# Kernel optimization log

Hardware: AMD Instinct MI355X
Metric: run time of the kernel (lower is better)

The kernel has to match this reference:

```python
import jax, jax.numpy as jnp
import numpy as np

B = 4096      # graphs
N = 21        # nodes per graph (EEG electrodes)
CIN = 512
H1 = 1024
H2 = 1024
COUT = 512
R = 4         # SE reduction
RANK = 10     # nodevec rank
EPS = 1e-5
THRESH = 0.1


def setup_inputs() -> dict:
    key = jax.random.key(0)
    ks = jax.random.split(key, 16)
    p = lambda i, shape, s=0.02: (jax.random.normal(ks[i], shape, jnp.float32) * s)
    return {
        "x": jax.random.normal(ks[0], (B * N, CIN), jnp.float32),
        "batch": jnp.arange(B * N, dtype=jnp.int32) // N,
        "nodevec1": jax.random.normal(ks[1], (N, RANK), jnp.float32),
        "nodevec2": jax.random.normal(ks[2], (RANK, N), jnp.float32),
        "se_w1": p(3, (CIN, CIN // R), 0.05),
        "se_w2": p(4, (CIN // R, CIN), 0.05),
        "W1": p(5, (CIN, H1)), "b1": jnp.zeros((H1,), jnp.float32),
        "W2": p(6, (H1, H2)), "b2": jnp.zeros((H2,), jnp.float32),
        "W3": p(7, (H2, COUT)), "b3": jnp.zeros((COUT,), jnp.float32),
        "bn1_g": jnp.ones((H1,), jnp.float32), "bn1_b": jnp.zeros((H1,), jnp.float32),
        "bn2_g": jnp.ones((H2,), jnp.float32), "bn2_b": jnp.zeros((H2,), jnp.float32),
        "bn3_g": jnp.ones((COUT,), jnp.float32), "bn3_b": jnp.zeros((COUT,), jnp.float32),
        "rs1_w": p(8, (CIN, H1)), "rs1_b": jnp.zeros((H1,), jnp.float32),
        "fc_w": p(9, (COUT, 2 * COUT)), "fc_b": jnp.zeros((2 * COUT,), jnp.float32),
    }


def _batchnorm(h, g, b):
    # training-mode BN: biased batch stats over the node dimension
    m = h.mean(0)
    v = h.var(0)
    return (h - m) * jax.lax.rsqrt(v + EPS) * g + b


def _gcn(A, h, W, b):
    # GCNConv with precomputed normalized+thresholded weights:
    # out = A_block_diag @ (h @ W) + b, done densely per graph since A is 21x21
    hm = (h @ W).reshape(B, N, -1)                 # [B, N, Cout]
    agg = jnp.einsum('ij,bjc->bic', A, hm)         # message passing per graph
    return agg.reshape(B * N, -1) + b


def _forward(x, batch, nodevec1, nodevec2, se_w1, se_w2,
             W1, b1, W2, b2, W3, b3,
             bn1_g, bn1_b, bn2_g, bn2_b, bn3_g, bn3_b,
             rs1_w, rs1_b, fc_w, fc_b):
    # SE layer on [B, N, C]: channel-wise gating from node-mean features
    x3 = x.reshape(B, N, CIN)
    y = jax.nn.sigmoid(jax.nn.relu(x3.mean(1) @ se_w1) @ se_w2)   # [B, C]
    xg = (x3 * y[:, None, :]).reshape(B * N, CIN)
    # adaptive adjacency: sigmoid(nv1 @ nv2), symmetric normalize, threshold
    adp = jax.nn.sigmoid(nodevec1 @ nodevec2)                      # [N, N]
    at = adp + jnp.eye(N, dtype=adp.dtype)
    deg = at.sum(1)
    dinv = jnp.where(deg > 0, deg ** -0.5, 0.0)
    A = dinv[:, None] * at * dinv[None, :]
    A = jnp.where(A > THRESH, A, 0.0)
    # layer 1 (+ projected residual, BN, relu; dropout omitted = eval)
    h = _batchnorm(_gcn(A, xg, W1, b1), bn1_g, bn1_b) + (xg @ rs1_w + rs1_b)
    h = jax.nn.relu(h)
    # layer 2 (h1 == h2 -> identity residual)
    h = jax.nn.relu(_batchnorm(_gcn(A, h, W2, b2), bn2_g, bn2_b) + h)
    # layer 3
    h = _batchnorm(_gcn(A, h, W3, b3), bn3_g, bn3_b)
    # global mean pool by graph id
    ssum = jax.ops.segment_sum(h, batch, num_segments=B)
    cnt = jax.ops.segment_sum(jnp.ones((h.shape[0], 1), h.dtype), batch, num_segments=B)
    pooled = ssum / cnt
    return pooled @ fc_w + fc_b                                    # [B, 2*COUT]


def reference(x, batch, nodevec1, nodevec2, se_w1, se_w2,
              W1, b1, W2, b2, W3, b3,
              bn1_g, bn1_b, bn2_g, bn2_b, bn3_g, bn3_b,
              rs1_w, rs1_b, fc_w, fc_b):
    return _forward(x, batch, nodevec1, nodevec2, se_w1, se_w2,
                    W1, b1, W2, b2, W3, b3,
                    bn1_g, bn1_b, bn2_g, bn2_b, bn3_g, bn3_b,
                    rs1_w, rs1_b, fc_w, fc_b)
```

## Files before the change

### kernel.cpp

```cpp
#include <hip/hip_runtime.h>

typedef _Float16 f16;
typedef f16 f16x2 __attribute__((ext_vector_type(2)));
typedef f16 f16x4 __attribute__((ext_vector_type(4)));
typedef f16 f16x8 __attribute__((ext_vector_type(8)));
typedef float f32x4 __attribute__((ext_vector_type(4)));
typedef const void __attribute__((address_space(1)))* gas1;
typedef void __attribute__((address_space(3)))* las3;

#define NB 4096
#define NN 21
#define MROWS (NB*NN)
#define CIN 512

__global__ void k_adj(const float* __restrict__ nv1, const float* __restrict__ nv2,
                      float* __restrict__ Aout) {
  __shared__ float at[21][21];
  __shared__ float dinv[21];
  int t = threadIdx.x;
  if (t < 441) {
    int i = t / 21, j = t % 21;
    float s = 0.f;
    #pragma unroll
    for (int r = 0; r < 10; r++) s += nv1[i*10 + r] * nv2[r*21 + j];
    float v = 1.f / (1.f + expf(-s));
    if (i == j) v += 1.f;
    at[i][j] = v;
  }
  __syncthreads();
  if (t < 21) {
    float d = 0.f;
    #pragma unroll
    for (int j = 0; j < 21; j++) d += at[t][j];
    dinv[t] = d > 0.f ? rsqrtf(d) : 0.f;
  }
  __syncthreads();
  if (t < 441) {
    int i = t / 21, j = t % 21;
    float a = dinv[i] * at[i][j] * dinv[j];
    Aout[t] = a > 0.1f ? a : 0.f;
  }
}

__global__ void k_transpose(const float* __restrict__ src, f16* __restrict__ dst,
                            int K, int N) {
  __shared__ float tile[32][33];
  int n0 = blockIdx.x * 32, k0 = blockIdx.y * 32;
  int tx = threadIdx.x, ty = threadIdx.y;
  #pragma unroll
  for (int i = 0; i < 4; i++)
    tile[ty + 8*i][tx] = src[(size_t)(k0 + ty + 8*i) * N + n0 + tx];
  __syncthreads();
  #pragma unroll
  for (int i = 0; i < 4; i++)
    dst[(size_t)(n0 + ty + 8*i) * K + k0 + tx] = (f16)tile[tx][ty + 8*i];
}

__global__ void k_mean(const float* __restrict__ x, float* __restrict__ xm) {
  int b = blockIdx.x, t = threadIdx.x;
  for (int c = t; c < CIN; c += 256) {
    float s = 0.f;
    #pragma unroll
    for (int n = 0; n < NN; n++) s += x[((size_t)b*NN + n)*CIN + c];
    xm[(size_t)b*CIN + c] = s * (1.f/21.f);
  }
}

__global__ void k_se1(const float* __restrict__ xm, const float* __restrict__ w1,
                      float* __restrict__ y1) {
  __shared__ float row[CIN];
  int b = blockIdx.x, t = threadIdx.x;
  for (int k = t; k < CIN; k += 128) row[k] = xm[(size_t)b*CIN + k];
  __syncthreads();
  float acc = 0.f;
  for (int k = 0; k < CIN; k++) acc += row[k] * w1[(size_t)k*128 + t];
  y1[(size_t)b*128 + t] = fmaxf(acc, 0.f);
}

__global__ void k_se2(const float* __restrict__ y1, const float* __restrict__ w2,
                      float* __restrict__ y) {
  __shared__ float row[128];
  int b = blockIdx.x, t = threadIdx.x;
  if (t < 128) row[t] = y1[(size_t)b*128 + t];
  __syncthreads();
  float acc = 0.f;
  for (int k = 0; k < 128; k++) acc += row[k] * w2[(size_t)k*CIN + t];
  y[(size_t)b*CIN + t] = 1.f / (1.f + expf(-acc));
}

__global__ void k_gate(const float* __restrict__ x, const float* __restrict__ y,
                       f16* __restrict__ xg) {
  size_t i8 = (size_t)blockIdx.x * 256 + threadIdx.x;
  size_t base = i8 * 8;
  int r = (int)(base >> 9);
  int c = (int)(base & 511);
  int b = r / 21;
  const float4* xp = (const float4*)(x + base);
  const float4* yp = (const float4*)(y + (size_t)b*CIN + c);
  float4 a0 = xp[0], a1 = xp[1];
  float4 g0 = yp[0], g1 = yp[1];
  f16x8 o;
  o[0] = (f16)(a0.x * g0.x); o[1] = (f16)(a0.y * g0.y);
  o[2] = (f16)(a0.z * g0.z); o[3] = (f16)(a0.w * g0.w);
  o[4] = (f16)(a1.x * g1.x); o[5] = (f16)(a1.y * g1.y);
  o[6] = (f16)(a1.z * g1.z); o[7] = (f16)(a1.w * g1.w);
  *(f16x8*)(xg + base) = o;
}

#define QBUF 65536

template<int MODE>
__global__ __launch_bounds__(512, 1)
void k_gemm256(const f16* __restrict__ A, const f16* __restrict__ BT,
               f16* __restrict__ C1, const float* __restrict__ bias,
               float* __restrict__ Cf, float* __restrict__ psum,
               float* __restrict__ psq, int N, int K, int lgn) {
  __shared__ __align__(16) char lds[2 * QBUF];
  const int tid = threadIdx.x;
  const int nwg = gridDim.x;
  const int g = blockIdx.x;
  const int swz = (g & 7) * (nwg >> 3) + (g >> 3);
  const int bn = swz & ((1 << lgn) - 1);
  const int bm = swz >> lgn;
  const int lane = tid & 63;
  const int wid = tid >> 6;
  const int wr = wid >> 2;
  const int wc = wid & 3;
  const int fr = lane & 15;
  const int kg = lane >> 4;

  int srcOff[8];
  #pragma unroll
  for (int j = 0; j < 8; j++) {
    int gid = j * 512 + tid;
    int row = (gid >> 3) & 255;
    int gr = gid & 7;
    int gsw = gr ^ (row & 7);
    srcOff[j] = ((j < 4 ? bm : bn) * 256 + row) * K + gsw * 8;
  }
  const int ldsBase = tid * 16;

  const int x7 = fr & 7;
  const int aBase = (wr*128 + fr) * 128;
  const int bBase = 32768 + (wc*64 + fr) * 128;

  f32x4 acc[8][4];
  #pragma unroll
  for (int m = 0; m < 8; m++)
    #pragma unroll
    for (int n = 0; n < 4; n++)
      #pragma unroll
      for (int r = 0; r < 4; r++) acc[m][n][r] = 0.f;

  auto STAGEH = [&](int t2, int sbuf, int j0) {
    char* dst = (char*)lds + sbuf * QBUF;
    const size_t kof = (size_t)t2 * 64;
    #pragma unroll
    for (int j = j0; j < j0 + 2; j++) {
      const f16* src = (j < 4 ? A : BT) + srcOff[j] + kof;
      __builtin_amdgcn_global_load_lds((gas1)src, (las3)(dst + ldsBase + j*8192), 16, 0, 0);
    }
  };
  auto READF = [&](f16x8* av, f16x8* bv, const char* rb, int s) {
    const int ko = ((s*4 + kg) ^ x7) << 4;
    #pragma unroll
    for (int m = 0; m < 8; m++) av[m] = *(const f16x8*)(rb + aBase + m*2048 + ko);
    #pragma unroll
    for (int n = 0; n < 4; n++) bv[n] = *(const f16x8*)(rb + bBase + n*2048 + ko);
  };

  f16x8 av[8], bv[4];
  const int NT = K >> 6;
  STAGEH(0, 0, 0); STAGEH(0, 0, 2); STAGEH(0, 0, 4); STAGEH(0, 0, 6);
  asm volatile("s_waitcnt vmcnt(0)" ::: "memory");
  asm volatile("s_barrier" ::: "memory");

  for (int t = 0; t < NT; t++) {
    const char* rb = (const char*)lds + (t & 1) * QBUF;
    const int nb = (t + 1) & 1;
    const bool stg = (t + 1) < NT;

    if (stg) { STAGEH(t + 1, nb, 0); STAGEH(t + 1, nb, 2); }
    READF(av, bv, rb, 0);
    __builtin_amdgcn_s_setprio(1);
    #pragma unroll
    for (int m = 0; m < 8; m++)
      #pragma unroll
      for (int n = 0; n < 4; n++)
        acc[m][n] = __builtin_amdgcn_mfma_f32_16x16x32_f16(bv[n], av[m], acc[m][n], 0, 0, 0);
    __builtin_amdgcn_s_setprio(0);
    if (stg) { STAGEH(t + 1, nb, 4); STAGEH(t + 1, nb, 6); }
    READF(av, bv, rb, 1);
    __builtin_amdgcn_s_setprio(1);
    #pragma unroll
    for (int m = 0; m < 8; m++)
      #pragma unroll
      for (int n = 0; n < 4; n++)
        acc[m][n] = __builtin_amdgcn_mfma_f32_16x16x32_f16(bv[n], av[m], acc[m][n], 0, 0, 0);
    __builtin_amdgcn_s_setprio(0);
    if (stg) asm volatile("s_waitcnt vmcnt(0)" ::: "memory");
    asm volatile("s_barrier" ::: "memory");
  }

  const int crow = bm*256 + wr*128 + fr;
  const int ccol = bn*256 + wc*64 + kg*4;
  if constexpr (MODE == 2) {
    #pragma unroll
    for (int n = 0; n < 4; n++) {
      float4 bb = *(const float4*)(bias + ccol + n*16);
      #pragma unroll
      for (int m = 0; m < 8; m++) {
        float4 v;
        v.x = acc[m][n][0] + bb.x; v.y = acc[m][n][1] + bb.y;
        v.z = acc[m][n][2] + bb.z; v.w = acc[m][n][3] + bb.w;
        *(float4*)(Cf + (size_t)(crow + m*16) * N + ccol + n*16) = v;
      }
    }
  } else {
    #pragma unroll
    for (int m = 0; m < 8; m++)
      #pragma unroll
      for (int n = 0; n < 4; n++) {
        f16x4 o;
        o[0] = (f16)acc[m][n][0]; o[1] = (f16)acc[m][n][1];
        o[2] = (f16)acc[m][n][2]; o[3] = (f16)acc[m][n][3];
        *(f16x4*)(C1 + (size_t)(crow + m*16) * N + ccol + n*16) = o;
      }
  }
  if constexpr (MODE == 1) {
    float s[4][4], q[4][4];
    #pragma unroll
    for (int n = 0; n < 4; n++)
      #pragma unroll
      for (int r = 0; r < 4; r++) {
        float ss = 0.f, qq = 0.f;
        #pragma unroll
        for (int m = 0; m < 8; m++) { float v = acc[m][n][r]; ss += v; qq = fmaf(v, v, qq); }
        s[n][r] = ss; q[n][r] = qq;
      }
    #pragma unroll
    for (int n = 0; n < 4; n++)
      #pragma unroll
      for (int r = 0; r < 4; r++) {
        s[n][r] += __shfl_xor(s[n][r], 1); s[n][r] += __shfl_xor(s[n][r], 2);
        s[n][r] += __shfl_xor(s[n][r], 4); s[n][r] += __shfl_xor(s[n][r], 8);
        q[n][r] += __shfl_xor(q[n][r], 1); q[n][r] += __shfl_xor(q[n][r], 2);
        q[n][r] += __shfl_xor(q[n][r], 4); q[n][r] += __shfl_xor(q[n][r], 8);
      }
    float* wred = (float*)lds;
    __syncthreads();
    if (fr == 0) {
      #pragma unroll
      for (int n = 0; n < 4; n++)
        #pragma unroll
        for (int r = 0; r < 4; r++) {
          int c = wc*64 + n*16 + kg*4 + r;
          wred[wr*256 + c]       = s[n][r];
          wred[512 + wr*256 + c] = q[n][r];
        }
    }
    __syncthreads();
    if (tid < 256) {
      psum[(size_t)bm * N + bn*256 + tid] = wred[tid]       + wred[256 + tid];
      psq [(size_t)bm * N + bn*256 + tid] = wred[512 + tid] + wred[768 + tid];
    }
  }
}

__global__ __launch_bounds__(256)
void k_mixip(f16* __restrict__ t, const float* __restrict__ Aadj) {
  __shared__ float A[441];
  int b = blockIdx.x, tid = threadIdx.x;
  for (int i = tid; i < 441; i += 256) A[i] = Aadj[i];
  __syncthreads();
  int c0 = tid * 2;
  size_t base = (size_t)b * NN * 512 + c0;
  float vx[21], vy[21];
  #pragma unroll
  for (int j = 0; j < 21; j++) {
    f16x2 v = *(const f16x2*)(t + base + (size_t)j * 512);
    vx[j] = (float)v[0]; vy[j] = (float)v[1];
  }
  #pragma unroll
  for (int i = 0; i < 21; i++) {
    float a0 = 0.f, a1 = 0.f;
    #pragma unroll
    for (int j = 0; j < 21; j++) { float w = A[i*21+j]; a0 = fmaf(w, vx[j], a0); a1 = fmaf(w, vy[j], a1); }
    f16x2 o; o[0] = (f16)a0; o[1] = (f16)a1;
    *(f16x2*)(t + base + (size_t)i * 512) = o;
  }
}

__global__ __launch_bounds__(256)
void k_mix(f16* __restrict__ t, const float* __restrict__ Aadj,
           float* __restrict__ psum, float* __restrict__ psq, int C) {
  __shared__ float A[441];
  int b = blockIdx.x, tid = threadIdx.x;
  for (int i = tid; i < 441; i += 256) A[i] = Aadj[i];
  __syncthreads();
  int c0 = (blockIdx.y * 256 + tid) * 2;
  size_t base = (size_t)b * NN * C + c0;
  float vx[21], vy[21];
  #pragma unroll
  for (int j = 0; j < 21; j++) {
    f16x2 v = *(const f16x2*)(t + base + (size_t)j * C);
    vx[j] = (float)v[0]; vy[j] = (float)v[1];
  }
  float s0 = 0.f, s1 = 0.f, q0 = 0.f, q1 = 0.f;
  #pragma unroll
  for (int i = 0; i < 21; i++) {
    float a0 = 0.f, a1 = 0.f;
    #pragma unroll
    for (int j = 0; j < 21; j++) {
      float w = A[i*21 + j];
      a0 = fmaf(w, vx[j], a0);
      a1 = fmaf(w, vy[j], a1);
    }
    f16x2 o; o[0] = (f16)a0; o[1] = (f16)a1;
    *(f16x2*)(t + base + (size_t)i * C) = o;
    s0 += a0; s1 += a1;
    q0 = fmaf(a0, a0, q0); q1 = fmaf(a1, a1, q1);
  }
  float2 sv; sv.x = s0; sv.y = s1;
  float2 qv; qv.x = q0; qv.y = q1;
  *(float2*)(psum + (size_t)b * C + c0) = sv;
  *(float2*)(psq  + (size_t)b * C + c0) = qv;
}

__global__ void k_reduce(const float* __restrict__ ps, const float* __restrict__ pq,
                         float* __restrict__ rs, float* __restrict__ rq,
                         int C, int per) {
  int c = blockIdx.x * 256 + threadIdx.x;
  int py = blockIdx.y;
  float s = 0.f, q = 0.f;
  for (int p = py*per; p < py*per + per; p++) {
    s += ps[(size_t)p*C + c];
    q += pq[(size_t)p*C + c];
  }
  rs[(size_t)py*C + c] = s;
  rq[(size_t)py*C + c] = q;
}

__global__ void k_bnparams(const float* __restrict__ psum, const float* __restrict__ psq,
                           const float* __restrict__ gamma, const float* __restrict__ beta,
                           const float* __restrict__ resbias,
                           float* __restrict__ scale, float* __restrict__ shift,
                           int C, int npart) {
  int c = blockIdx.x * 256 + threadIdx.x;
  float s = 0.f, q = 0.f;
  for (int p = 0; p < npart; p++) { s += psum[(size_t)p*C + c]; q += psq[(size_t)p*C + c]; }
  const float Minv = 1.f / (float)MROWS;
  float mean = s * Minv;
  float var = q * Minv - mean * mean;
  float sc = gamma[c] * rsqrtf(var + 1e-5f);
  float sh = beta[c] - mean * sc;
  if (resbias) sh += resbias[c];
  scale[c] = sc; shift[c] = sh;
}

__global__ void k_finalize(const f16* __restrict__ g, const f16* res,
                           f16* dst, const float* __restrict__ scale,
                           const float* __restrict__ shift, int cmask) {
  size_t i8 = (size_t)blockIdx.x * 256 + threadIdx.x;
  size_t base = i8 * 8;
  int c = (int)(base & (size_t)cmask);
  f16x8 gv = *(const f16x8*)(g + base);
  f16x8 rv = *(const f16x8*)(res + base);
  f16x8 o;
  #pragma unroll
  for (int j = 0; j < 8; j++) {
    float v = (float)gv[j] * scale[c + j] + shift[c + j] + (float)rv[j];
    o[j] = (f16)fmaxf(v, 0.f);
  }
  *(f16x8*)(dst + base) = o;
}

__global__ __launch_bounds__(256)
void k_finmix(const f16* t, const f16* res, f16* hout, f16* hmix,
              const float* __restrict__ scale, const float* __restrict__ shift,
              const float* __restrict__ Aadj, int C) {
  __shared__ float A[441];
  int b = blockIdx.x, tid = threadIdx.x;
  for (int i = tid; i < 441; i += 256) A[i] = Aadj[i];
  __syncthreads();
  int c0 = (blockIdx.y * 256 + tid) * 2;
  float scx = scale[c0], scy = scale[c0+1];
  float shx = shift[c0], shy = shift[c0+1];
  size_t base = (size_t)b * NN * C + c0;
  float hx[21], hy[21];
  #pragma unroll
  for (int j = 0; j < 21; j++) {
    f16x2 tv = *(const f16x2*)(t + base + (size_t)j*C);
    f16x2 rv = *(const f16x2*)(res + base + (size_t)j*C);
    hx[j] = fmaxf((float)tv[0]*scx + shx + (float)rv[0], 0.f);
    hy[j] = fmaxf((float)tv[1]*scy + shy + (float)rv[1], 0.f);
    if (hout) {
      f16x2 o; o[0] = (f16)hx[j]; o[1] = (f16)hy[j];
      *(f16x2*)(hout + base + (size_t)j*C) = o;
    }
  }
  #pragma unroll
  for (int i = 0; i < 21; i++) {
    float a0 = 0.f, a1 = 0.f;
    #pragma unroll
    for (int j = 0; j < 21; j++) { float w = A[i*21+j]; a0 = fmaf(w, hx[j], a0); a1 = fmaf(w, hy[j], a1); }
    f16x2 o; o[0] = (f16)a0; o[1] = (f16)a1;
    *(f16x2*)(hmix + base + (size_t)i*C) = o;
  }
}

__global__ void k_pool(const f16* __restrict__ g3, const float* __restrict__ scale,
                       const float* __restrict__ shift, f16* __restrict__ pooled) {
  int b = blockIdx.x, t = threadIdx.x;
  for (int c = t; c < 512; c += 256) {
    float s = 0.f;
    #pragma unroll
    for (int n = 0; n < NN; n++) s += (float)g3[((size_t)b*NN + n)*512 + c];
    pooled[(size_t)b*512 + c] = (f16)((s * (1.f/21.f)) * scale[c] + shift[c]);
  }
}

extern "C" void kernel_launch(void* const* d_in, const int* in_sizes, int n_in,
                              void* d_out, int out_size, void* d_ws, size_t ws_size,
                              hipStream_t stream) {
  const float* x     = (const float*)d_in[0];
  const float* nv1   = (const float*)d_in[2];
  const float* nv2   = (const float*)d_in[3];
  const float* se_w1 = (const float*)d_in[4];
  const float* se_w2 = (const float*)d_in[5];
  const float* W1    = (const float*)d_in[6];
  const float* W2    = (const float*)d_in[8];
  const float* W3    = (const float*)d_in[10];
  const float* bn1g  = (const float*)d_in[12];
  const float* bn1b  = (const float*)d_in[13];
  const float* bn2g  = (const float*)d_in[14];
  const float* bn2b  = (const float*)d_in[15];
  const float* bn3g  = (const float*)d_in[16];
  const float* bn3b  = (const float*)d_in[17];
  const float* rs1w  = (const float*)d_in[18];
  const float* rs1b  = (const float*)d_in[19];
  const float* fcw   = (const float*)d_in[20];
  const float* fcb   = (const float*)d_in[21];
  float* out = (float*)d_out;

  char* ws = (char*)d_ws;
  size_t off = 0;
  auto alloc = [&](size_t bytes) -> char* {
    char* p = ws + off;
    off = (off + bytes + 255) & ~(size_t)255;
    return p;
  };

  float* A_adj = (float*)alloc(441 * 4);
  f16* W1T  = (f16*)alloc((size_t)1024 * 512 * 2);
  f16* RS1T = (f16*)alloc((size_t)1024 * 512 * 2);
  f16* W2T  = (f16*)alloc((size_t)1024 * 1024 * 2);
  f16* W3T  = (f16*)alloc((size_t)512 * 1024 * 2);
  f16* FCWT = (f16*)alloc((size_t)1024 * 512 * 2);
  float* psum = (float*)alloc((size_t)NB * 1024 * 4);
  float* psq  = (float*)alloc((size_t)NB * 1024 * 4);
  float* y1   = (float*)alloc((size_t)NB * 128 * 4);
  float* rsum = (float*)alloc((size_t)32 * 1024 * 4);
  float* rsq  = (float*)alloc((size_t)32 * 1024 * 4);
  float* sc1 = (float*)alloc(1024 * 4);
  float* sh1 = (float*)alloc(1024 * 4);
  float* sc2 = (float*)alloc(1024 * 4);
  float* sh2 = (float*)alloc(1024 * 4);
  float* sc3 = (float*)alloc(1024 * 4);
  float* sh3 = (float*)alloc(1024 * 4);
  f16* pooled = (f16*)alloc((size_t)NB * 512 * 2);
  f16* G = (f16*)alloc((size_t)MROWS * 512 * 2);
  f16* R = (f16*)alloc((size_t)MROWS * 1024 * 2);
  f16* T = (f16*)alloc((size_t)MROWS * 1024 * 2);
  float* xm = psum;
  float* yv = psq;
  (void)ws_size; (void)in_sizes; (void)n_in; (void)out_size;

  k_adj<<<1, 512, 0, stream>>>(nv1, nv2, A_adj);
  k_transpose<<<dim3(32, 16), dim3(32, 8), 0, stream>>>(W1,   W1T,  512, 1024);
  k_transpose<<<dim3(32, 16), dim3(32, 8), 0, stream>>>(rs1w, RS1T, 512, 1024);
  k_transpose<<<dim3(32, 32), dim3(32, 8), 0, stream>>>(W2,   W2T,  1024, 1024);
  k_transpose<<<dim3(16, 32), dim3(32, 8), 0, stream>>>(W3,   W3T,  1024, 512);
  k_transpose<<<dim3(32, 16), dim3(32, 8), 0, stream>>>(fcw,  FCWT, 512, 1024);

  k_mean<<<NB, 256, 0, stream>>>(x, xm);
  k_se1<<<NB, 128, 0, stream>>>(xm, se_w1, y1);
  k_se2<<<NB, 512, 0, stream>>>(y1, se_w2, yv);
  k_gate<<<21504, 256, 0, stream>>>(x, yv, G);

  k_gemm256<0><<<1344, 512, 0, stream>>>(G, RS1T, R, nullptr, nullptr, nullptr, nullptr, 1024, 512, 2);
  k_mixip<<<NB, 256, 0, stream>>>(G, A_adj);
  k_gemm256<1><<<1344, 512, 0, stream>>>(G, W1T, T, nullptr, nullptr, psum, psq, 1024, 512, 2);
  k_reduce<<<dim3(4, 24), 256, 0, stream>>>(psum, psq, rsum, rsq, 1024, 14);
  k_bnparams<<<4, 256, 0, stream>>>(rsum, rsq, bn1g, bn1b, rs1b, sc1, sh1, 1024, 24);
  k_finalize<<<43008, 256, 0, stream>>>(T, R, R, sc1, sh1, 1023);

  k_gemm256<0><<<1344, 512, 0, stream>>>(R, W2T, T, nullptr, nullptr, nullptr, nullptr, 1024, 1024, 2);
  k_mix<<<dim3(NB, 2), 256, 0, stream>>>(T, A_adj, psum, psq, 1024);
  k_reduce<<<dim3(4, 32), 256, 0, stream>>>(psum, psq, rsum, rsq, 1024, 128);
  k_bnparams<<<4, 256, 0, stream>>>(rsum, rsq, bn2g, bn2b, nullptr, sc2, sh2, 1024, 32);
  k_finmix<<<dim3(NB, 2), 256, 0, stream>>>(T, R, nullptr, T, sc2, sh2, A_adj, 1024);

  k_gemm256<1><<<672, 512, 0, stream>>>(T, W3T, G, nullptr, nullptr, psum, psq, 512, 1024, 1);
  k_reduce<<<dim3(2, 24), 256, 0, stream>>>(psum, psq, rsum, rsq, 512, 14);
  k_bnparams<<<2, 256, 0, stream>>>(rsum, rsq, bn3g, bn3b, nullptr, sc3, sh3, 512, 24);

  k_pool<<<NB, 256, 0, stream>>>(G, sc3, sh3, pooled);
  k_gemm256<2><<<64, 512, 0, stream>>>(pooled, FCWT, nullptr, fcb, out, nullptr, nullptr, 1024, 512, 2);
}
```

Baseline: 1.180 ms.

## Fuse SE mean/MLP/gate into one kernel and batch weight transposes

Replaces the four SE kernels (mean, two small MLP layers, gate) with one kernel that processes 8 graphs per block. Per-graph means and MLP activations stay in shared memory, and the w1/w2 weight loads are shared across the 8 graphs. The five weight-transpose launches become a single launch that picks its matrix by block index. For layers 1 and 3, the separate reduce step is dropped and the BN-parameter kernel sums all 336 partials directly, which cuts launches but makes each of only 2–4 blocks do a long serial loop. The SE kernel reads x twice and runs only 512 blocks, so occupancy may be lower.

```diff
diff --git a/kernel.cpp b/kernel.cpp
--- a/kernel.cpp
+++ b/kernel.cpp
@@ -42,10 +42,22 @@
   }
 }
 
-__global__ void k_transpose(const float* __restrict__ src, f16* __restrict__ dst,
-                            int K, int N) {
+__global__ void k_transpose_all(const float* __restrict__ s0, const float* __restrict__ s1,
+                                const float* __restrict__ s2, const float* __restrict__ s3,
+                                const float* __restrict__ s4,
+                                f16* __restrict__ d0, f16* __restrict__ d1,
+                                f16* __restrict__ d2, f16* __restrict__ d3,
+                                f16* __restrict__ d4) {
   __shared__ float tile[32][33];
-  int n0 = blockIdx.x * 32, k0 = blockIdx.y * 32;
+  int b = blockIdx.x;
+  const float* src; f16* dst; int K, N, local;
+  if (b < 512)       { src = s0; dst = d0; K = 512;  N = 1024; local = b; }
+  else if (b < 1024) { src = s1; dst = d1; K = 512;  N = 1024; local = b - 512; }
+  else if (b < 2048) { src = s2; dst = d2; K = 1024; N = 1024; local = b - 1024; }
+  else if (b < 2560) { src = s3; dst = d3; K = 1024; N = 512;  local = b - 2048; }
+  else               { src = s4; dst = d4; K = 512;  N = 1024; local = b - 2560; }
+  int ntn = N >> 5;
+  int n0 = (local % ntn) * 32, k0 = (local / ntn) * 32;
   int tx = threadIdx.x, ty = threadIdx.y;
   #pragma unroll
   for (int i = 0; i < 4; i++)
@@ -56,55 +68,74 @@
     dst[(size_t)(n0 + ty + 8*i) * K + k0 + tx] = (f16)tile[tx][ty + 8*i];
 }
 
-__global__ void k_mean(const float* __restrict__ x, float* __restrict__ xm) {
-  int b = blockIdx.x, t = threadIdx.x;
-  for (int c = t; c < CIN; c += 256) {
-    float s = 0.f;
-    #pragma unroll
-    for (int n = 0; n < NN; n++) s += x[((size_t)b*NN + n)*CIN + c];
-    xm[(size_t)b*CIN + c] = s * (1.f/21.f);
-  }
-}
-
-__global__ void k_se1(const float* __restrict__ xm, const float* __restrict__ w1,
-                      float* __restrict__ y1) {
-  __shared__ float row[CIN];
-  int b = blockIdx.x, t = threadIdx.x;
-  for (int k = t; k < CIN; k += 128) row[k] = xm[(size_t)b*CIN + k];
-  __syncthreads();
-  float acc = 0.f;
-  for (int k = 0; k < CIN; k++) acc += row[k] * w1[(size_t)k*128 + t];
-  y1[(size_t)b*128 + t] = fmaxf(acc, 0.f);
-}
-
-__global__ void k_se2(const float* __restrict__ y1, const float* __restrict__ w2,
-                      float* __restrict__ y) {
-  __shared__ float row[128];
-  int b = blockIdx.x, t = threadIdx.x;
-  if (t < 128) row[t] = y1[(size_t)b*128 + t];
-  __syncthreads();
-  float acc = 0.f;
-  for (int k = 0; k < 128; k++) acc += row[k] * w2[(size_t)k*CIN + t];
-  y[(size_t)b*CIN + t] = 1.f / (1.f + expf(-acc));
-}
-
-__global__ void k_gate(const float* __restrict__ x, const float* __restrict__ y,
-                       f16* __restrict__ xg) {
-  size_t i8 = (size_t)blockIdx.x * 256 + threadIdx.x;
-  size_t base = i8 * 8;
-  int r = (int)(base >> 9);
-  int c = (int)(base & 511);
-  int b = r / 21;
-  const float4* xp = (const float4*)(x + base);
-  const float4* yp = (const float4*)(y + (size_t)b*CIN + c);
-  float4 a0 = xp[0], a1 = xp[1];
-  float4 g0 = yp[0], g1 = yp[1];
-  f16x8 o;
-  o[0] = (f16)(a0.x * g0.x); o[1] = (f16)(a0.y * g0.y);
-  o[2] = (f16)(a0.z * g0.z); o[3] = (f16)(a0.w * g0.w);
-  o[4] = (f16)(a1.x * g1.x); o[5] = (f16)(a1.y * g1.y);
-  o[6] = (f16)(a1.z * g1.z); o[7] = (f16)(a1.w * g1.w);
-  *(f16x8*)(xg + base) = o;
+__global__ __launch_bounds__(256)
+void k_segate(const float* __restrict__ x, const float* __restrict__ w1,
+              const float* __restrict__ w2, f16* __restrict__ xg) {
+  __shared__ float xm[8][512];
+  __shared__ float y1[8][128];
+  __shared__ float yv[8][512];
+  const int tid = threadIdx.x;
+  const int g0 = blockIdx.x * 8;
+  const int c0 = tid * 2;
+  for (int i = 0; i < 8; i++) {
+    const float* xb = x + ((size_t)(g0 + i) * NN) * 512 + c0;
+    float s0 = 0.f, s1 = 0.f;
+    #pragma unroll
+    for (int n = 0; n < NN; n++) {
+      float2 v = *(const float2*)(xb + (size_t)n * 512);
+      s0 += v.x; s1 += v.y;
+    }
+    xm[i][c0]   = s0 * (1.f/21.f);
+    xm[i][c0+1] = s1 * (1.f/21.f);
+  }
+  __syncthreads();
+  {
+    int o = tid & 127, ih = tid >> 7;
+    float a0 = 0.f, a1 = 0.f, a2 = 0.f, a3 = 0.f;
+    for (int k = 0; k < 512; k++) {
+      float w = w1[k*128 + o];
+      a0 = fmaf(xm[ih  ][k], w, a0);
+      a1 = fmaf(xm[ih+2][k], w, a1);
+      a2 = fmaf(xm[ih+4][k], w, a2);
+      a3 = fmaf(xm[ih+6][k], w, a3);
+    }
+    y1[ih  ][o] = fmaxf(a0, 0.f);
+    y1[ih+2][o] = fmaxf(a1, 0.f);
+    y1[ih+4][o] = fmaxf(a2, 0.f);
+    y1[ih+6][o] = fmaxf(a3, 0.f);
+  }
+  __syncthreads();
+  {
+    float acc[8][2];
+    #pragma unroll
+    for (int i = 0; i < 8; i++) { acc[i][0] = 0.f; acc[i][1] = 0.f; }
+    for (int j = 0; j < 128; j++) {
+      float wa = w2[j*512 + tid];
+      float wb = w2[j*512 + tid + 256];
+      #pragma unroll
+      for (int i = 0; i < 8; i++) {
+        float yj = y1[i][j];
+        acc[i][0] = fmaf(yj, wa, acc[i][0]);
+        acc[i][1] = fmaf(yj, wb, acc[i][1]);
+      }
+    }
+    #pragma unroll
+    for (int i = 0; i < 8; i++) {
+      yv[i][tid]       = 1.f / (1.f + expf(-acc[i][0]));
+      yv[i][tid + 256] = 1.f / (1.f + expf(-acc[i][1]));
+    }
+  }
+  __syncthreads();
+  for (int i = 0; i < 8; i++) {
+    float ga = yv[i][c0], gb = yv[i][c0+1];
+    size_t base = ((size_t)(g0 + i) * NN) * 512 + c0;
+    #pragma unroll
+    for (int n = 0; n < NN; n++) {
+      float2 v = *(const float2*)(x + base + (size_t)n * 512);
+      f16x2 o2; o2[0] = (f16)(v.x * ga); o2[1] = (f16)(v.y * gb);
+      *(f16x2*)(xg + base + (size_t)n * 512) = o2;
+    }
+  }
 }
 
 #define QBUF 65536
@@ -341,11 +372,11 @@
   rq[(size_t)py*C + c] = q;
 }
 
-__global__ void k_bnparams(const float* __restrict__ psum, const float* __restrict__ psq,
-                           const float* __restrict__ gamma, const float* __restrict__ beta,
-                           const float* __restrict__ resbias,
-                           float* __restrict__ scale, float* __restrict__ shift,
-                           int C, int npart) {
+__global__ void k_bnfuse(const float* __restrict__ psum, const float* __restrict__ psq,
+                         const float* __restrict__ gamma, const float* __restrict__ beta,
+                         const float* __restrict__ resbias,
+                         float* __restrict__ scale, float* __restrict__ shift,
+                         int C, int npart) {
   int c = blockIdx.x * 256 + threadIdx.x;
   float s = 0.f, q = 0.f;
   for (int p = 0; p < npart; p++) { s += psum[(size_t)p*C + c]; q += psq[(size_t)p*C + c]; }
@@ -459,7 +490,6 @@
   f16* FCWT = (f16*)alloc((size_t)1024 * 512 * 2);
   float* psum = (float*)alloc((size_t)NB * 1024 * 4);
   float* psq  = (float*)alloc((size_t)NB * 1024 * 4);
-  float* y1   = (float*)alloc((size_t)NB * 128 * 4);
   float* rsum = (float*)alloc((size_t)32 * 1024 * 4);
   float* rsq  = (float*)alloc((size_t)32 * 1024 * 4);
   float* sc1 = (float*)alloc(1024 * 4);
@@ -472,38 +502,28 @@
   f16* G = (f16*)alloc((size_t)MROWS * 512 * 2);
   f16* R = (f16*)alloc((size_t)MROWS * 1024 * 2);
   f16* T = (f16*)alloc((size_t)MROWS * 1024 * 2);
-  float* xm = psum;
-  float* yv = psq;
   (void)ws_size; (void)in_sizes; (void)n_in; (void)out_size;
 
   k_adj<<<1, 512, 0, stream>>>(nv1, nv2, A_adj);
-  k_transpose<<<dim3(32, 16), dim3(32, 8), 0, stream>>>(W1,   W1T,  512, 1024);
-  k_transpose<<<dim3(32, 16), dim3(32, 8), 0, stream>>>(rs1w, RS1T, 512, 1024);
-  k_transpose<<<dim3(32, 32), dim3(32, 8), 0, stream>>>(W2,   W2T,  1024, 1024);
-  k_transpose<<<dim3(16, 32), dim3(32, 8), 0, stream>>>(W3,   W3T,  1024, 512);
-  k_transpose<<<dim3(32, 16), dim3(32, 8), 0, stream>>>(fcw,  FCWT, 512, 1024);
-
-  k_mean<<<NB, 256, 0, stream>>>(x, xm);
-  k_se1<<<NB, 128, 0, stream>>>(xm, se_w1, y1);
-  k_se2<<<NB, 512, 0, stream>>>(y1, se_w2, yv);
-  k_gate<<<21504, 256, 0, stream>>>(x, yv, G);
+  k_transpose_all<<<3072, dim3(32, 8), 0, stream>>>(W1, rs1w, W2, W3, fcw,
+                                                    W1T, RS1T, W2T, W3T, FCWT);
+
+  k_segate<<<512, 256, 0, stream>>>(x, se_w1, se_w2, G);
 
   k_gemm256<0><<<1344, 512, 0, stream>>>(G, RS1T, R, nullptr, nullptr, nullptr, nullptr, 1024, 512, 2);
   k_mixip<<<NB, 256, 0, stream>>>(G, A_adj);
   k_gemm256<1><<<1344, 512, 0, stream>>>(G, W1T, T, nullptr, nullptr, psum, psq, 1024, 512, 2);
-  k_reduce<<<dim3(4, 24), 256, 0, stream>>>(psum, psq, rsum, rsq, 1024, 14);
-  k_bnparams<<<4, 256, 0, stream>>>(rsum, rsq, bn1g, bn1b, rs1b, sc1, sh1, 1024, 24);
+  k_bnfuse<<<4, 256, 0, stream>>>(psum, psq, bn1g, bn1b, rs1b, sc1, sh1, 1024, 336);
   k_finalize<<<43008, 256, 0, stream>>>(T, R, R, sc1, sh1, 1023);
 
   k_gemm256<0><<<1344, 512, 0, stream>>>(R, W2T, T, nullptr, nullptr, nullptr, nullptr, 1024, 1024, 2);
   k_mix<<<dim3(NB, 2), 256, 0, stream>>>(T, A_adj, psum, psq, 1024);
   k_reduce<<<dim3(4, 32), 256, 0, stream>>>(psum, psq, rsum, rsq, 1024, 128);
-  k_bnparams<<<4, 256, 0, stream>>>(rsum, rsq, bn2g, bn2b, nullptr, sc2, sh2, 1024, 32);
+  k_bnfuse<<<4, 256, 0, stream>>>(rsum, rsq, bn2g, bn2b, nullptr, sc2, sh2, 1024, 32);
   k_finmix<<<dim3(NB, 2), 256, 0, stream>>>(T, R, nullptr, T, sc2, sh2, A_adj, 1024);
 
   k_gemm256<1><<<672, 512, 0, stream>>>(T, W3T, G, nullptr, nullptr, psum, psq, 512, 1024, 1);
-  k_reduce<<<dim3(2, 24), 256, 0, stream>>>(psum, psq, rsum, rsq, 512, 14);
-  k_bnparams<<<2, 256, 0, stream>>>(rsum, rsq, bn3g, bn3b, nullptr, sc3, sh3, 512, 24);
+  k_bnfuse<<<2, 256, 0, stream>>>(psum, psq, bn3g, bn3b, nullptr, sc3, sh3, 512, 336);
 
   k_pool<<<NB, 256, 0, stream>>>(G, sc3, sh3, pooled);
   k_gemm256<2><<<64, 512, 0, stream>>>(pooled, FCWT, nullptr, fcb, out, nullptr, nullptr, 1024, 512, 2);
```

After: 1.279 ms. +8.4%, slower.
